# Performance work log

Hardware: AMD Instinct MI355X
Metric: run time of the kernel (lower is better)

## Reference

```python
import jax, jax.numpy as jnp
import numpy as np


def setup_inputs() -> dict:
    key = jax.random.key(0)
    B, C, L = 32, 64, 8192
    x = jax.random.normal(key, (B, C, L), dtype=jnp.float32)
    return {"x": x, "kernel_size": 9}


def reference(x, kernel_size):
    # Sliding-window median along the last (time) axis with replicate padding,
    # matching nn.ReplicationPad1d + Unfold + torch.median (lower median; k is odd
    # so it is the exact median = k//2-th order statistic).
    k = kernel_size
    p = (k - 1) // 2
    L = x.shape[-1]
    xp = jnp.pad(x, ((0, 0), (0, 0), (p, p)), mode="edge")  # [B, C, L + k - 1]
    # Stack the k shifted views -> [B, C, L, k] (k is a small static constant)
    win = jnp.stack([xp[:, :, i:i + L] for i in range(k)], axis=-1)
    return jnp.sort(win, axis=-1)[..., k // 2]
```

## Files before the change

### kernel.cpp

```cpp
#include <hip/hip_runtime.h>


#define TILE 1024
#define BLOCK 256
#define HALO 4

__device__ __forceinline__ float med3(float a, float b, float c) {
    return __builtin_amdgcn_fmed3f(a, b, c);
}
__device__ __forceinline__ float min3(float a, float b, float c) {
    return fminf(fminf(a, b), c);
}
__device__ __forceinline__ float max3(float a, float b, float c) {
    return fmaxf(fmaxf(a, b), c);
}

__device__ __forceinline__ float med9(float p0, float p1, float p2,
                                      float p3, float p4, float p5,
                                      float p6, float p7, float p8) {
    float l0 = min3(p0, p1, p2), m0 = med3(p0, p1, p2), h0 = max3(p0, p1, p2);
    float l1 = min3(p3, p4, p5), m1 = med3(p3, p4, p5), h1 = max3(p3, p4, p5);
    float l2 = min3(p6, p7, p8), m2 = med3(p6, p7, p8), h2 = max3(p6, p7, p8);
    return med3(max3(l0, l1, l2), med3(m0, m1, m2), min3(h0, h1, h2));
}

__global__ __launch_bounds__(BLOCK) void median9_kernel(
    const float* __restrict__ x, float* __restrict__ out, int L, int tilesPerRow) {
    __shared__ __align__(16) float s[TILE + 2 * HALO];

    const int tid = threadIdx.x;
    const int row = blockIdx.x / tilesPerRow;
    const int tile_start = (blockIdx.x % tilesPerRow) * TILE;
    const long long row_base = (long long)row * L;
    const float* xr = x + row_base;

    float4 v = ((const float4*)(xr + tile_start))[tid];
    ((float4*)(s + HALO))[tid] = v;

    if (tid < 2 * HALO) {
        int pos, sidx;
        if (tid < HALO) {
            pos = tile_start - HALO + tid;
            sidx = tid;
        } else {
            pos = tile_start + TILE + (tid - HALO);
            sidx = TILE + HALO + (tid - HALO);
        }
        pos = min(max(pos, 0), L - 1);
        s[sidx] = xr[pos];
    }
    __syncthreads();

    const float4* sv = (const float4*)(s + 4 * tid);
    float4 a = sv[0], b = sv[1], c = sv[2];

    float4 r;
    r.x = med9(a.x, a.y, a.z, a.w, b.x, b.y, b.z, b.w, c.x);
    r.y = med9(a.y, a.z, a.w, b.x, b.y, b.z, b.w, c.x, c.y);
    r.z = med9(a.z, a.w, b.x, b.y, b.z, b.w, c.x, c.y, c.z);
    r.w = med9(a.w, b.x, b.y, b.z, b.w, c.x, c.y, c.z, c.w);

    ((float4*)(out + row_base + tile_start))[tid] = r;
}

extern "C" void kernel_launch(void* const* d_in, const int* in_sizes, int n_in,
                              void* d_out, int out_size, void* d_ws, size_t ws_size,
                              hipStream_t stream) {
    const float* x = (const float*)d_in[0];
    float* out = (float*)d_out;
    const int L = 8192;
    const int rows = in_sizes[0] / L;
    const int tilesPerRow = L / TILE;
    const int nblocks = rows * tilesPerRow;
    median9_kernel<<<nblocks, BLOCK, 0, stream>>>(x, out, L, tilesPerRow);
}
```

Baseline: 113.7 us.

## Replace shared-memory tiling with direct halo float4 loads, 8 outputs per thread

Drops the LDS staging buffer and __syncthreads. Each thread now loads its own 8 elements plus left and right float4 halos straight from global memory, using replicate padding at the row edges. Each thread computes 8 medians instead of 4, and tiles double to 2048 elements, which halves the block count. Neighbouring halo loads are re-read through the cache rather than shared, adding some redundant global traffic, but this should be absorbed by L2.

```diff
diff --git a/kernel.cpp b/kernel.cpp
--- a/kernel.cpp
+++ b/kernel.cpp
@@ -1,9 +1,9 @@
 #include <hip/hip_runtime.h>
 
 
-#define TILE 1024
 #define BLOCK 256
-#define HALO 4
+#define OPT 8
+#define TILE (BLOCK * OPT)
 
 __device__ __forceinline__ float med3(float a, float b, float c) {
     return __builtin_amdgcn_fmed3f(a, b, c);
@@ -26,41 +26,45 @@
 
 __global__ __launch_bounds__(BLOCK) void median9_kernel(
     const float* __restrict__ x, float* __restrict__ out, int L, int tilesPerRow) {
-    __shared__ __align__(16) float s[TILE + 2 * HALO];
-
     const int tid = threadIdx.x;
     const int row = blockIdx.x / tilesPerRow;
-    const int tile_start = (blockIdx.x % tilesPerRow) * TILE;
-    const long long row_base = (long long)row * L;
-    const float* xr = x + row_base;
+    const int col0 = (blockIdx.x % tilesPerRow) * TILE + tid * OPT;
+    const float* p = x + (long long)row * L + col0;
 
-    float4 v = ((const float4*)(xr + tile_start))[tid];
-    ((float4*)(s + HALO))[tid] = v;
+    float4 A4 = ((const float4*)p)[0];
+    float4 B4 = ((const float4*)p)[1];
 
-    if (tid < 2 * HALO) {
-        int pos, sidx;
-        if (tid < HALO) {
-            pos = tile_start - HALO + tid;
-            sidx = tid;
-        } else {
-            pos = tile_start + TILE + (tid - HALO);
-            sidx = TILE + HALO + (tid - HALO);
-        }
-        pos = min(max(pos, 0), L - 1);
-        s[sidx] = xr[pos];
+    float4 L4;
+    if (col0 == 0) {
+        L4 = make_float4(A4.x, A4.x, A4.x, A4.x);
+    } else {
+        L4 = *(const float4*)(p - 4);
     }
-    __syncthreads();
+    float4 R4;
+    if (col0 + OPT == L) {
+        R4 = make_float4(B4.w, B4.w, B4.w, B4.w);
+    } else {
+        R4 = *(const float4*)(p + 8);
+    }
 
-    const float4* sv = (const float4*)(s + 4 * tid);
-    float4 a = sv[0], b = sv[1], c = sv[2];
+    float s0 = L4.x, s1 = L4.y, s2 = L4.z, s3 = L4.w;
+    float s4 = A4.x, s5 = A4.y, s6 = A4.z, s7 = A4.w;
+    float s8 = B4.x, s9 = B4.y, s10 = B4.z, s11 = B4.w;
+    float s12 = R4.x, s13 = R4.y, s14 = R4.z, s15 = R4.w;
 
-    float4 r;
-    r.x = med9(a.x, a.y, a.z, a.w, b.x, b.y, b.z, b.w, c.x);
-    r.y = med9(a.y, a.z, a.w, b.x, b.y, b.z, b.w, c.x, c.y);
-    r.z = med9(a.z, a.w, b.x, b.y, b.z, b.w, c.x, c.y, c.z);
-    r.w = med9(a.w, b.x, b.y, b.z, b.w, c.x, c.y, c.z, c.w);
+    float4 r0, r1;
+    r0.x = med9(s0, s1, s2, s3, s4, s5, s6, s7, s8);
+    r0.y = med9(s1, s2, s3, s4, s5, s6, s7, s8, s9);
+    r0.z = med9(s2, s3, s4, s5, s6, s7, s8, s9, s10);
+    r0.w = med9(s3, s4, s5, s6, s7, s8, s9, s10, s11);
+    r1.x = med9(s4, s5, s6, s7, s8, s9, s10, s11, s12);
+    r1.y = med9(s5, s6, s7, s8, s9, s10, s11, s12, s13);
+    r1.z = med9(s6, s7, s8, s9, s10, s11, s12, s13, s14);
+    r1.w = med9(s7, s8, s9, s10, s11, s12, s13, s14, s15);
 
-    ((float4*)(out + row_base + tile_start))[tid] = r;
+    float* o = out + (long long)row * L + col0;
+    ((float4*)o)[0] = r0;
+    ((float4*)o)[1] = r1;
 }
 
 extern "C" void kernel_launch(void* const* d_in, const int* in_sizes, int n_in,
```

Result: no change. 115.9 us (+2.0%).
